# Kernel optimization log

Hardware: AMD Instinct MI355X
Metric: run time of the kernel (lower is better)

Reference implementation:

```python
import jax, jax.numpy as jnp
import numpy as np

B, Lq, Lkv = 4, 1024, 4096
Cq, Ckv, E, NH = 512, 512, 512, 8
HD = E // NH


def setup_inputs() -> dict:
    key = jax.random.key(0)
    ks = jax.random.split(key, 8)
    s = 0.02
    return {
        "Xq": jax.random.normal(ks[0], (B, Lq, Cq), dtype=jnp.float32),
        "Xkv": jax.random.normal(ks[1], (B, Lkv, Ckv), dtype=jnp.float32),
        "mask": jax.random.randint(ks[2], (B, Lq, 1), 0, 2, dtype=jnp.int32),
        "Wq": jax.random.normal(ks[3], (Cq, E), dtype=jnp.float32) * s,
        "bq": jnp.zeros((E,), dtype=jnp.float32),
        "Wkv": jax.random.normal(ks[4], (Ckv, 2 * E), dtype=jnp.float32) * s,
        "bkv": jnp.zeros((2 * E,), dtype=jnp.float32),
        "Wp": jax.random.normal(ks[5], (E, E), dtype=jnp.float32) * s,
        "bp": jnp.zeros((E,), dtype=jnp.float32),
        "attn_pos": jax.random.normal(ks[6], (1, NH, Lq, Lkv), dtype=jnp.float32) * s,
    }


def reference(Xq, Xkv, mask, Wq, bq, Wkv, bkv, Wp, bp, attn_pos):
    scale = HD ** -0.5
    # projections
    Q = (Xq @ Wq + bq).reshape(B, Lq, NH, HD).transpose(0, 2, 1, 3) * scale  # [B,NH,Lq,HD]
    KV = (Xkv @ Wkv + bkv).reshape(B, Lkv, 2, NH, HD)
    K = KV[:, :, 0].transpose(0, 2, 1, 3)  # [B,NH,Lkv,HD]
    V = KV[:, :, 1].transpose(0, 2, 1, 3)
    # scores + learned positional bias
    attn = jnp.einsum('bhqd,bhkd->bhqk', Q, K) + attn_pos  # [B,NH,Lq,Lkv]
    # dummy-column masked softmax (mask: [B,Lq,1], 1=keep row)
    m = mask.astype(attn.dtype)[:, None]           # [B,1,Lq,1]
    attn = attn + (1.0 - m) * (-100.0)             # suppress masked query rows
    dummy = jnp.broadcast_to(jnp.where(m == 0, 100.0, -100.0), (B, NH, Lq, 1))
    attn = jax.nn.softmax(jnp.concatenate([attn, dummy], axis=-1), axis=-1)[..., :Lkv]
    # weighted sum + output projection (dropout = identity in eval)
    out = jnp.einsum('bhqk,bhkd->bhqd', attn, V)
    out = out.transpose(0, 2, 1, 3).reshape(B, Lq, E)
    return out @ Wp + bp
```

## Files before the change

### kernel.cpp

```cpp
#include <hip/hip_runtime.h>

typedef unsigned short u16;
typedef __attribute__((ext_vector_type(8))) short bf16x8;
typedef __attribute__((ext_vector_type(4))) float f32x4;
typedef __attribute__((ext_vector_type(2))) unsigned u32x2;

__device__ __forceinline__ u16 f2bf(float x) {
    union { float f; unsigned u; } v; v.f = x;
    unsigned r = v.u + 0x7FFF + ((v.u >> 16) & 1);
    return (u16)(r >> 16);
}

__device__ __forceinline__ unsigned cvt_pk_bf16(float lo, float hi) {
    unsigned r;
    asm("v_cvt_pk_bf16_f32 %0, %1, %2" : "=v"(r) : "v"(lo), "v"(hi));
    return r;
}

__global__ __launch_bounds__(256) void transpose_w(const float* __restrict__ in,
                                                   u16* __restrict__ out, int R, int C) {
    __shared__ float tile[64][65];
    int r0 = blockIdx.y * 64, c0 = blockIdx.x * 64;
    int tid = threadIdx.x;
#pragma unroll
    for (int j = 0; j < 16; ++j) {
        int e = tid + j * 256;
        int row = e >> 6, col = e & 63;
        tile[row][col] = in[(size_t)(r0 + row) * C + c0 + col];
    }
    __syncthreads();
#pragma unroll
    for (int j = 0; j < 16; ++j) {
        int e = tid + j * 256;
        int row = e >> 6, col = e & 63;
        out[(size_t)(c0 + row) * R + r0 + col] = f2bf(tile[col][row]);
    }
}

__global__ __launch_bounds__(256) void transpose_v(const u16* __restrict__ in,
                                                   u16* __restrict__ out) {
    __shared__ u16 tile[64][65];
    int bh = blockIdx.y;
    int r0 = blockIdx.x * 64;
    const u16* ip = in + (size_t)bh * 4096 * 64;
    u16* op = out + (size_t)bh * 64 * 4096;
    int tid = threadIdx.x;
#pragma unroll
    for (int j = 0; j < 16; ++j) {
        int e = tid + j * 256;
        int row = e >> 6, col = e & 63;
        tile[row][col] = ip[(size_t)(r0 + row) * 64 + col];
    }
    __syncthreads();
#pragma unroll
    for (int j = 0; j < 16; ++j) {
        int e = tid + j * 256;
        int row = e >> 6, col = e & 63;
        op[(size_t)row * 4096 + r0 + col] = tile[col][row];
    }
}

template <int MODE>
__global__ __launch_bounds__(256) void gemm_kernel(const void* __restrict__ Aptr,
                                                   const u16* __restrict__ Bt,
                                                   const float* __restrict__ bias,
                                                   void* __restrict__ Cout,
                                                   void* __restrict__ Cout2,
                                                   int M, int N, int K) {
    __shared__ u16 Al[128][40];
    __shared__ u16 Bl[128][40];
    int tid = threadIdx.x;
    int lane = tid & 63, wid = tid >> 6;
    int wr = wid >> 1, wc = wid & 1;
    int l15 = lane & 15, g = lane >> 4;
    int bm = blockIdx.y, bn = blockIdx.x;

    f32x4 acc[4][4];
#pragma unroll
    for (int m = 0; m < 4; ++m)
#pragma unroll
        for (int n = 0; n < 4; ++n)
#pragma unroll
            for (int j = 0; j < 4; ++j) acc[m][n][j] = 0.f;

    int nK = K >> 5;
    for (int kt = 0; kt < nK; ++kt) {
        __syncthreads();
        if (MODE != 2) {
            const float* A = (const float*)Aptr;
#pragma unroll
            for (int j = 0; j < 4; ++j) {
                int idx4 = tid + j * 256;
                int row = idx4 >> 3, c4 = (idx4 & 7) << 2;
                const float4* p =
                    (const float4*)(A + (size_t)(bm * 128 + row) * K + kt * 32 + c4);
                float4 v = *p;
                u32x2 w = {cvt_pk_bf16(v.x, v.y), cvt_pk_bf16(v.z, v.w)};
                *(u32x2*)&Al[row][c4] = w;
            }
        } else {
            const u16* A = (const u16*)Aptr;
#pragma unroll
            for (int j = 0; j < 2; ++j) {
                int idx8 = tid + j * 256;
                int row = idx8 >> 2, c8 = (idx8 & 3) << 3;
                bf16x8 v = *(const bf16x8*)(A + (size_t)(bm * 128 + row) * K + kt * 32 + c8);
                *(bf16x8*)&Al[row][c8] = v;
            }
        }
#pragma unroll
        for (int j = 0; j < 2; ++j) {
            int idx8 = tid + j * 256;
            int row = idx8 >> 2, c8 = (idx8 & 3) << 3;
            bf16x8 v = *(const bf16x8*)(Bt + (size_t)(bn * 128 + row) * K + kt * 32 + c8);
            *(bf16x8*)&Bl[row][c8] = v;
        }
        __syncthreads();

        bf16x8 af[4], bfr[4];
#pragma unroll
        for (int m = 0; m < 4; ++m) af[m] = *(const bf16x8*)&Al[wr * 64 + m * 16 + l15][g * 8];
#pragma unroll
        for (int n = 0; n < 4; ++n) bfr[n] = *(const bf16x8*)&Bl[wc * 64 + n * 16 + l15][g * 8];
#pragma unroll
        for (int m = 0; m < 4; ++m)
#pragma unroll
            for (int n = 0; n < 4; ++n)
                acc[m][n] =
                    __builtin_amdgcn_mfma_f32_16x16x32_bf16(af[m], bfr[n], acc[m][n], 0, 0, 0);
    }

#pragma unroll
    for (int m = 0; m < 4; ++m)
#pragma unroll
        for (int n = 0; n < 4; ++n)
#pragma unroll
            for (int j = 0; j < 4; ++j) {
                int row = bm * 128 + wr * 64 + m * 16 + g * 4 + j;
                int col = bn * 128 + wc * 64 + n * 16 + l15;
                float v = acc[m][n][j] + bias[col];
                if (MODE == 0) {
                    int b = row >> 10, q = row & 1023, h = col >> 6, d = col & 63;
                    ((u16*)Cout)[(((size_t)((b * 8 + h) * 1024 + q)) << 6) + d] =
                        f2bf(v * 0.125f);
                } else if (MODE == 1) {
                    int b = row >> 12, kv = row & 4095;
                    int d = col & 63;
                    if (col < 512) {
                        int h = col >> 6;
                        ((u16*)Cout)[(((size_t)((b * 8 + h) * 4096 + kv)) << 6) + d] = f2bf(v);
                    } else {
                        int h = (col - 512) >> 6;
                        ((u16*)Cout2)[(((size_t)((b * 8 + h) * 4096 + kv)) << 6) + d] = f2bf(v);
                    }
                } else {
                    ((float*)Cout)[(size_t)row * N + col] = v;
                }
            }
}

__global__ __launch_bounds__(256, 3) void attn_kernel(const u16* __restrict__ Qb,
                                                      const u16* __restrict__ Kb,
                                                      const u16* __restrict__ Vt,
                                                      const float* __restrict__ pos,
                                                      float* __restrict__ Opart,
                                                      float* __restrict__ Lp) {
    __shared__ u16 Klds[64][72];
    __shared__ u16 Vlds[64][72];
    __shared__ u16 Plds[4][32][72];

    int idx = blockIdx.x;
    int bh = idx & 31;
    int zz = idx >> 5;
    int qt = zz & 7, sp = zz >> 3;
    int b = bh >> 3, h = bh & 7;
    int q0 = qt * 128;
    int kvbase = sp * 512;
    int tid = threadIdx.x, lane = tid & 63, wid = tid >> 6;
    int l15 = lane & 15, g = lane >> 4;

    bf16x8 aq[2][2];
#pragma unroll
    for (int m = 0; m < 2; ++m) {
        const u16* qp =
            Qb + (((size_t)((b * 8 + h) * 1024 + q0 + wid * 32 + m * 16 + l15)) << 6) + g * 8;
        aq[m][0] = *(const bf16x8*)(qp);
        aq[m][1] = *(const bf16x8*)(qp + 32);
    }

    f32x4 o[2][4];
    f32x4 lacc[2];
#pragma unroll
    for (int m = 0; m < 2; ++m) {
#pragma unroll
        for (int j = 0; j < 4; ++j) lacc[m][j] = 0.f;
#pragma unroll
        for (int n = 0; n < 4; ++n)
#pragma unroll
            for (int j = 0; j < 4; ++j) o[m][n][j] = 0.f;
    }

    const size_t kbase = ((size_t)(b * 8 + h)) * 4096 * 64;
    const float* posp =
        pos + (size_t)h * 1024 * 4096 + (size_t)(q0 + wid * 32 + g * 4) * 4096 + kvbase;

    int srow = tid >> 3, sc8 = (tid & 7) << 3;

    bf16x8 kr[2], vr[2];
    f32x4 zr[2][4];
#pragma unroll
    for (int j = 0; j < 2; ++j) {
        int row = srow + j * 32;
        kr[j] = *(const bf16x8*)(Kb + kbase + (size_t)(kvbase + row) * 64 + sc8);
        vr[j] = *(const bf16x8*)(Vt + kbase + (size_t)row * 4096 + kvbase + sc8);
    }
#pragma unroll
    for (int m = 0; m < 2; ++m)
#pragma unroll
        for (int n = 0; n < 4; ++n)
#pragma unroll
            for (int j = 0; j < 4; ++j)
                zr[m][n][j] = posp[(size_t)(m * 16 + j) * 4096 + n * 16 + l15];

    const short one_s = (short)0x3F80;
    bf16x8 ones = {one_s, one_s, one_s, one_s, one_s, one_s, one_s, one_s};

    for (int kt = 0; kt < 8; ++kt) {
        __syncthreads();
#pragma unroll
        for (int j = 0; j < 2; ++j) {
            int row = srow + j * 32;
            *(bf16x8*)&Klds[row][sc8] = kr[j];
            *(bf16x8*)&Vlds[row][sc8] = vr[j];
        }
        __syncthreads();

        int knext = (kt + 1) & 7;
#pragma unroll
        for (int j = 0; j < 2; ++j) {
            int row = srow + j * 32;
            kr[j] = *(const bf16x8*)(Kb + kbase + (size_t)(kvbase + knext * 64 + row) * 64 + sc8);
            vr[j] = *(const bf16x8*)(Vt + kbase + (size_t)row * 4096 + kvbase + knext * 64 + sc8);
        }

        f32x4 s[2][4];
        __builtin_amdgcn_s_setprio(1);
#pragma unroll
        for (int n = 0; n < 4; ++n) {
            bf16x8 kb0 = *(const bf16x8*)&Klds[n * 16 + l15][g * 8];
            bf16x8 kb1 = *(const bf16x8*)&Klds[n * 16 + l15][32 + g * 8];
#pragma unroll
            for (int m = 0; m < 2; ++m) {
                f32x4 t =
                    __builtin_amdgcn_mfma_f32_16x16x32_bf16(aq[m][0], kb0, zr[m][n], 0, 0, 0);
                s[m][n] = __builtin_amdgcn_mfma_f32_16x16x32_bf16(aq[m][1], kb1, t, 0, 0, 0);
            }
        }
        __builtin_amdgcn_s_setprio(0);

#pragma unroll
        for (int m = 0; m < 2; ++m)
#pragma unroll
            for (int n = 0; n < 4; ++n)
#pragma unroll
                for (int j = 0; j < 4; ++j)
                    zr[m][n][j] = posp[(size_t)(m * 16 + j) * 4096 + knext * 64 + n * 16 + l15];

#pragma unroll
        for (int m = 0; m < 2; ++m)
#pragma unroll
            for (int n = 0; n < 4; ++n)
#pragma unroll
                for (int j = 0; j < 4; ++j)
                    s[m][n][j] = __builtin_exp2f(fminf(s[m][n][j], 60.f) * 1.44269504f);

#pragma unroll
        for (int m = 0; m < 2; ++m)
#pragma unroll
            for (int j = 0; j < 4; ++j) {
                unsigned w0 = cvt_pk_bf16(s[m][0][j], s[m][1][j]);
                unsigned w1 = cvt_pk_bf16(s[m][2][j], s[m][3][j]);
                int row = m * 16 + g * 4 + j;
                Plds[wid][row][l15] = (u16)w0;
                Plds[wid][row][16 + l15] = (u16)(w0 >> 16);
                Plds[wid][row][32 + l15] = (u16)w1;
                Plds[wid][row][48 + l15] = (u16)(w1 >> 16);
            }
        asm volatile("" ::: "memory");

        bf16x8 pa[2][2];
#pragma unroll
        for (int m = 0; m < 2; ++m) {
            pa[m][0] = *(const bf16x8*)&Plds[wid][m * 16 + l15][g * 8];
            pa[m][1] = *(const bf16x8*)&Plds[wid][m * 16 + l15][32 + g * 8];
        }

        __builtin_amdgcn_s_setprio(1);
#pragma unroll
        for (int n = 0; n < 4; ++n) {
            bf16x8 vb0 = *(const bf16x8*)&Vlds[n * 16 + l15][g * 8];
            bf16x8 vb1 = *(const bf16x8*)&Vlds[n * 16 + l15][32 + g * 8];
#pragma unroll
            for (int m = 0; m < 2; ++m) {
                o[m][n] = __builtin_amdgcn_mfma_f32_16x16x32_bf16(pa[m][0], vb0, o[m][n], 0, 0, 0);
                o[m][n] = __builtin_amdgcn_mfma_f32_16x16x32_bf16(pa[m][1], vb1, o[m][n], 0, 0, 0);
            }
        }
#pragma unroll
        for (int m = 0; m < 2; ++m) {
            lacc[m] = __builtin_amdgcn_mfma_f32_16x16x32_bf16(pa[m][0], ones, lacc[m], 0, 0, 0);
            lacc[m] = __builtin_amdgcn_mfma_f32_16x16x32_bf16(pa[m][1], ones, lacc[m], 0, 0, 0);
        }
        __builtin_amdgcn_s_setprio(0);
    }

    int obase = (sp * 32 + bh) * 1024;
#pragma unroll
    for (int m = 0; m < 2; ++m)
#pragma unroll
        for (int j = 0; j < 4; ++j) {
            int row = q0 + wid * 32 + m * 16 + g * 4 + j;
#pragma unroll
            for (int n = 0; n < 4; ++n)
                Opart[((size_t)(obase + row)) * 64 + n * 16 + l15] = o[m][n][j];
            if (l15 == 0) Lp[obase + row] = lacc[m][j];
        }
}

__global__ __launch_bounds__(256) void attn_combine(const float* __restrict__ Opart,
                                                    const float* __restrict__ Lp,
                                                    const int* __restrict__ mask,
                                                    u16* __restrict__ AO) {
    int tid = threadIdx.x;
    int d = tid & 63;
    int r = blockIdx.x * 4 + (tid >> 6);
    int bh = r >> 10, q = r & 1023;
    int b = bh >> 3, h = bh & 7;

    float L = 0.f, val = 0.f;
#pragma unroll
    for (int s2 = 0; s2 < 8; ++s2) {
        size_t rr = (size_t)(s2 * 32 + bh) * 1024 + q;
        L += Lp[rr];
        val += Opart[rr * 64 + d];
    }
    float res = mask[b * 1024 + q] ? (val / L) : 0.f;
    AO[((size_t)(b * 1024 + q)) * 512 + h * 64 + d] = f2bf(res);
}

extern "C" void kernel_launch(void* const* d_in, const int* in_sizes, int n_in,
                              void* d_out, int out_size, void* d_ws, size_t ws_size,
                              hipStream_t stream) {
    const float* Xq = (const float*)d_in[0];
    const float* Xkv = (const float*)d_in[1];
    const int* mask = (const int*)d_in[2];
    const float* Wq = (const float*)d_in[3];
    const float* bq = (const float*)d_in[4];
    const float* Wkv = (const float*)d_in[5];
    const float* bkv = (const float*)d_in[6];
    const float* Wp = (const float*)d_in[7];
    const float* bp = (const float*)d_in[8];
    const float* pos = (const float*)d_in[9];
    float* out = (float*)d_out;

    char* ws = (char*)d_ws;
    u16* WqT = (u16*)(ws);
    u16* WkvT = (u16*)(ws + 524288);
    u16* WpT = (u16*)(ws + 1572864);
    u16* Qb = (u16*)(ws + 2097152);
    u16* Kb = (u16*)(ws + 6291456);
    u16* Vt = (u16*)(ws + 23068672);
    u16* AO = (u16*)(ws + 39845888);
    float* Opart = (float*)(ws + 44040192);
    u16* Vtm = (u16*)(ws + 44040192);
    float* Lp = (float*)(ws + 111149056);

    transpose_w<<<dim3(8, 8), 256, 0, stream>>>(Wq, WqT, 512, 512);
    transpose_w<<<dim3(16, 8), 256, 0, stream>>>(Wkv, WkvT, 512, 1024);
    transpose_w<<<dim3(8, 8), 256, 0, stream>>>(Wp, WpT, 512, 512);
    gemm_kernel<0><<<dim3(4, 32), 256, 0, stream>>>(Xq, WqT, bq, Qb, nullptr, 4096, 512, 512);
    gemm_kernel<1><<<dim3(8, 128), 256, 0, stream>>>(Xkv, WkvT, bkv, Kb, Vtm, 16384, 1024, 512);
    transpose_v<<<dim3(64, 32), 256, 0, stream>>>(Vtm, Vt);
    attn_kernel<<<dim3(2048), 256, 0, stream>>>(Qb, Kb, Vt, pos, Opart, Lp);
    attn_combine<<<dim3(8192), 256, 0, stream>>>(Opart, Lp, mask, AO);
    gemm_kernel<2><<<dim3(4, 32), 256, 0, stream>>>(AO, WpT, bp, out, nullptr, 4096, 512, 512);
}
```

Measured before the change: 206.6 us.

## Pre-convert inputs to bf16, use direct global-to-LDS GEMM loads, transpose attention score layout

Adds a pre-pass that converts Xq and Xkv to bf16. The projection GEMMs now load A and B tiles straight into LDS with global_load_lds, using a 64-wide K step. The attention kernel swaps the MFMA operands so scores come out transposed, which allows vectorized f32x4 loads of the positional bias and a smaller P staging buffer written with packed stores. The log2e factor is folded into the Q scale and the bias, and occupancy is raised to 4 blocks per CU. This trades extra conversion kernels and workspace traffic for cheaper GEMM staging and fewer attention memory instructions. It risks LDS bank conflicts because the unpadded 64-wide tiles are read back with strided row accesses.

```diff
diff --git a/kernel.cpp b/kernel.cpp
--- a/kernel.cpp
+++ b/kernel.cpp
@@ -4,6 +4,7 @@
 typedef __attribute__((ext_vector_type(8))) short bf16x8;
 typedef __attribute__((ext_vector_type(4))) float f32x4;
 typedef __attribute__((ext_vector_type(2))) unsigned u32x2;
+typedef __attribute__((ext_vector_type(4))) unsigned u32x4;
 
 __device__ __forceinline__ u16 f2bf(float x) {
     union { float f; unsigned u; } v; v.f = x;
@@ -15,6 +16,21 @@
     unsigned r;
     asm("v_cvt_pk_bf16_f32 %0, %1, %2" : "=v"(r) : "v"(lo), "v"(hi));
     return r;
+}
+
+__device__ __forceinline__ void gl_lds16(const u16* g, u16* l) {
+    __builtin_amdgcn_global_load_lds((const __attribute__((address_space(1))) void*)g,
+                                     (__attribute__((address_space(3))) void*)l, 16, 0, 0);
+}
+
+__global__ __launch_bounds__(256) void conv_bf16(const float* __restrict__ in,
+                                                 u16* __restrict__ out) {
+    size_t i = ((size_t)blockIdx.x * 256 + threadIdx.x) * 8;
+    const float4* p = (const float4*)(in + i);
+    float4 a = p[0], b = p[1];
+    u32x4 w = {cvt_pk_bf16(a.x, a.y), cvt_pk_bf16(a.z, a.w),
+               cvt_pk_bf16(b.x, b.y), cvt_pk_bf16(b.z, b.w)};
+    *(u32x4*)(out + i) = w;
 }
 
 __global__ __launch_bounds__(256) void transpose_w(const float* __restrict__ in,
@@ -61,19 +77,20 @@
 }
 
 template <int MODE>
-__global__ __launch_bounds__(256) void gemm_kernel(const void* __restrict__ Aptr,
+__global__ __launch_bounds__(256) void gemm_kernel(const u16* __restrict__ A,
                                                    const u16* __restrict__ Bt,
                                                    const float* __restrict__ bias,
                                                    void* __restrict__ Cout,
                                                    void* __restrict__ Cout2,
                                                    int M, int N, int K) {
-    __shared__ u16 Al[128][40];
-    __shared__ u16 Bl[128][40];
+    __shared__ u16 Al[128][64];
+    __shared__ u16 Bl[128][64];
     int tid = threadIdx.x;
     int lane = tid & 63, wid = tid >> 6;
     int wr = wid >> 1, wc = wid & 1;
     int l15 = lane & 15, g = lane >> 4;
     int bm = blockIdx.y, bn = blockIdx.x;
+    int ldr = lane >> 3, ldc = (lane & 7) << 3;
 
     f32x4 acc[4][4];
 #pragma unroll
@@ -83,51 +100,34 @@
 #pragma unroll
             for (int j = 0; j < 4; ++j) acc[m][n][j] = 0.f;
 
-    int nK = K >> 5;
+    int nK = K >> 6;
     for (int kt = 0; kt < nK; ++kt) {
         __syncthreads();
-        if (MODE != 2) {
-            const float* A = (const float*)Aptr;
-#pragma unroll
-            for (int j = 0; j < 4; ++j) {
-                int idx4 = tid + j * 256;
-                int row = idx4 >> 3, c4 = (idx4 & 7) << 2;
-                const float4* p =
-                    (const float4*)(A + (size_t)(bm * 128 + row) * K + kt * 32 + c4);
-                float4 v = *p;
-                u32x2 w = {cvt_pk_bf16(v.x, v.y), cvt_pk_bf16(v.z, v.w)};
-                *(u32x2*)&Al[row][c4] = w;
-            }
-        } else {
-            const u16* A = (const u16*)Aptr;
-#pragma unroll
-            for (int j = 0; j < 2; ++j) {
-                int idx8 = tid + j * 256;
-                int row = idx8 >> 2, c8 = (idx8 & 3) << 3;
-                bf16x8 v = *(const bf16x8*)(A + (size_t)(bm * 128 + row) * K + kt * 32 + c8);
-                *(bf16x8*)&Al[row][c8] = v;
-            }
-        }
-#pragma unroll
-        for (int j = 0; j < 2; ++j) {
-            int idx8 = tid + j * 256;
-            int row = idx8 >> 2, c8 = (idx8 & 3) << 3;
-            bf16x8 v = *(const bf16x8*)(Bt + (size_t)(bn * 128 + row) * K + kt * 32 + c8);
-            *(bf16x8*)&Bl[row][c8] = v;
+#pragma unroll
+        for (int i = 0; i < 4; ++i) {
+            int c = wid * 4 + i;
+            int row = c * 8 + ldr;
+            gl_lds16(A + (size_t)(bm * 128 + row) * K + kt * 64 + ldc, &Al[0][0] + c * 512);
+            gl_lds16(Bt + (size_t)(bn * 128 + row) * K + kt * 64 + ldc, &Bl[0][0] + c * 512);
         }
         __syncthreads();
 
-        bf16x8 af[4], bfr[4];
-#pragma unroll
-        for (int m = 0; m < 4; ++m) af[m] = *(const bf16x8*)&Al[wr * 64 + m * 16 + l15][g * 8];
-#pragma unroll
-        for (int n = 0; n < 4; ++n) bfr[n] = *(const bf16x8*)&Bl[wc * 64 + n * 16 + l15][g * 8];
-#pragma unroll
-        for (int m = 0; m < 4; ++m)
+#pragma unroll
+        for (int kk = 0; kk < 2; ++kk) {
+            bf16x8 af[4], bfr[4];
+#pragma unroll
+            for (int m = 0; m < 4; ++m)
+                af[m] = *(const bf16x8*)&Al[wr * 64 + m * 16 + l15][kk * 32 + g * 8];
 #pragma unroll
             for (int n = 0; n < 4; ++n)
-                acc[m][n] =
-                    __builtin_amdgcn_mfma_f32_16x16x32_bf16(af[m], bfr[n], acc[m][n], 0, 0, 0);
+                bfr[n] = *(const bf16x8*)&Bl[wc * 64 + n * 16 + l15][kk * 32 + g * 8];
+#pragma unroll
+            for (int m = 0; m < 4; ++m)
+#pragma unroll
+                for (int n = 0; n < 4; ++n)
+                    acc[m][n] =
+                        __builtin_amdgcn_mfma_f32_16x16x32_bf16(af[m], bfr[n], acc[m][n], 0, 0, 0);
+        }
     }
 
 #pragma unroll
@@ -142,7 +142,7 @@
                 if (MODE == 0) {
                     int b = row >> 10, q = row & 1023, h = col >> 6, d = col & 63;
                     ((u16*)Cout)[(((size_t)((b * 8 + h) * 1024 + q)) << 6) + d] =
-                        f2bf(v * 0.125f);
+                        f2bf(v * 0.18033688011112042f);
                 } else if (MODE == 1) {
                     int b = row >> 12, kv = row & 4095;
                     int d = col & 63;
@@ -159,7 +159,7 @@
             }
 }
 
-__global__ __launch_bounds__(256, 3) void attn_kernel(const u16* __restrict__ Qb,
+__global__ __launch_bounds__(256, 4) void attn_kernel(const u16* __restrict__ Qb,
                                                       const u16* __restrict__ Kb,
                                                       const u16* __restrict__ Vt,
                                                       const float* __restrict__ pos,
@@ -167,7 +167,7 @@
                                                       float* __restrict__ Lp) {
     __shared__ u16 Klds[64][72];
     __shared__ u16 Vlds[64][72];
-    __shared__ u16 Plds[4][32][72];
+    __shared__ u16 Plds[4][16][72];
 
     int idx = blockIdx.x;
     int bh = idx & 31;
@@ -202,7 +202,7 @@
 
     const size_t kbase = ((size_t)(b * 8 + h)) * 4096 * 64;
     const float* posp =
-        pos + (size_t)h * 1024 * 4096 + (size_t)(q0 + wid * 32 + g * 4) * 4096 + kvbase;
+        pos + (size_t)h * 1024 * 4096 + (size_t)(q0 + wid * 32 + l15) * 4096 + kvbase;
 
     int srow = tid >> 3, sc8 = (tid & 7) << 3;
 
@@ -217,10 +217,11 @@
 #pragma unroll
     for (int m = 0; m < 2; ++m)
 #pragma unroll
-        for (int n = 0; n < 4; ++n)
-#pragma unroll
-            for (int j = 0; j < 4; ++j)
-                zr[m][n][j] = posp[(size_t)(m * 16 + j) * 4096 + n * 16 + l15];
+        for (int n = 0; n < 4; ++n) {
+            zr[m][n] = *(const f32x4*)(posp + (size_t)m * 16 * 4096 + n * 16 + g * 4);
+#pragma unroll
+            for (int j = 0; j < 4; ++j) zr[m][n][j] *= 1.44269504f;
+        }
 
     const short one_s = (short)0x3F80;
     bf16x8 ones = {one_s, one_s, one_s, one_s, one_s, one_s, one_s, one_s};
@@ -252,8 +253,8 @@
 #pragma unroll
             for (int m = 0; m < 2; ++m) {
                 f32x4 t =
-                    __builtin_amdgcn_mfma_f32_16x16x32_bf16(aq[m][0], kb0, zr[m][n], 0, 0, 0);
-                s[m][n] = __builtin_amdgcn_mfma_f32_16x16x32_bf16(aq[m][1], kb1, t, 0, 0, 0);
+                    __builtin_amdgcn_mfma_f32_16x16x32_bf16(kb0, aq[m][0], zr[m][n], 0, 0, 0);
+                s[m][n] = __builtin_amdgcn_mfma_f32_16x16x32_bf16(kb1, aq[m][1], t, 0, 0, 0);
             }
         }
         __builtin_amdgcn_s_setprio(0);
@@ -261,38 +262,35 @@
 #pragma unroll
         for (int m = 0; m < 2; ++m)
 #pragma unroll
+            for (int n = 0; n < 4; ++n) {
+                zr[m][n] = *(const f32x4*)(posp + (size_t)m * 16 * 4096 + knext * 64 + n * 16 +
+                                           g * 4);
+#pragma unroll
+                for (int j = 0; j < 4; ++j) zr[m][n][j] *= 1.44269504f;
+            }
+
+#pragma unroll
+        for (int m = 0; m < 2; ++m)
+#pragma unroll
             for (int n = 0; n < 4; ++n)
 #pragma unroll
                 for (int j = 0; j < 4; ++j)
-                    zr[m][n][j] = posp[(size_t)(m * 16 + j) * 4096 + knext * 64 + n * 16 + l15];
-
-#pragma unroll
-        for (int m = 0; m < 2; ++m)
-#pragma unroll
-            for (int n = 0; n < 4; ++n)
-#pragma unroll
-                for (int j = 0; j < 4; ++j)
-                    s[m][n][j] = __builtin_exp2f(fminf(s[m][n][j], 60.f) * 1.44269504f);
-
-#pragma unroll
-        for (int m = 0; m < 2; ++m)
-#pragma unroll
-            for (int j = 0; j < 4; ++j) {
-                unsigned w0 = cvt_pk_bf16(s[m][0][j], s[m][1][j]);
-                unsigned w1 = cvt_pk_bf16(s[m][2][j], s[m][3][j]);
-                int row = m * 16 + g * 4 + j;
-                Plds[wid][row][l15] = (u16)w0;
-                Plds[wid][row][16 + l15] = (u16)(w0 >> 16);
-                Plds[wid][row][32 + l15] = (u16)w1;
-                Plds[wid][row][48 + l15] = (u16)(w1 >> 16);
-            }
-        asm volatile("" ::: "memory");
+                    s[m][n][j] = __builtin_exp2f(fminf(s[m][n][j], 80.f));
 
         bf16x8 pa[2][2];
 #pragma unroll
         for (int m = 0; m < 2; ++m) {
-            pa[m][0] = *(const bf16x8*)&Plds[wid][m * 16 + l15][g * 8];
-            pa[m][1] = *(const bf16x8*)&Plds[wid][m * 16 + l15][32 + g * 8];
+#pragma unroll
+            for (int n = 0; n < 4; ++n) {
+                u32x2 w;
+                w.x = cvt_pk_bf16(s[m][n][0], s[m][n][1]);
+                w.y = cvt_pk_bf16(s[m][n][2], s[m][n][3]);
+                *(u32x2*)&Plds[wid][l15][n * 16 + g * 4] = w;
+            }
+            asm volatile("" ::: "memory");
+            pa[m][0] = *(const bf16x8*)&Plds[wid][l15][g * 8];
+            pa[m][1] = *(const bf16x8*)&Plds[wid][l15][32 + g * 8];
+            asm volatile("" ::: "memory");
         }
 
         __builtin_amdgcn_s_setprio(1);
@@ -372,14 +370,18 @@
     u16* Vt = (u16*)(ws + 23068672);
     u16* AO = (u16*)(ws + 39845888);
     float* Opart = (float*)(ws + 44040192);
-    u16* Vtm = (u16*)(ws + 44040192);
+    u16* Xkvb = (u16*)(ws + 44040192);
+    u16* Vtm = (u16*)(ws + 60817408);
+    u16* Xqb = (u16*)(ws + 77594624);
     float* Lp = (float*)(ws + 111149056);
 
+    conv_bf16<<<dim3(1024), 256, 0, stream>>>(Xq, Xqb);
+    conv_bf16<<<dim3(4096), 256, 0, stream>>>(Xkv, Xkvb);
     transpose_w<<<dim3(8, 8), 256, 0, stream>>>(Wq, WqT, 512, 512);
     transpose_w<<<dim3(16, 8), 256, 0, stream>>>(Wkv, WkvT, 512, 1024);
     transpose_w<<<dim3(8, 8), 256, 0, stream>>>(Wp, WpT, 512, 512);
-    gemm_kernel<0><<<dim3(4, 32), 256, 0, stream>>>(Xq, WqT, bq, Qb, nullptr, 4096, 512, 512);
-    gemm_kernel<1><<<dim3(8, 128), 256, 0, stream>>>(Xkv, WkvT, bkv, Kb, Vtm, 16384, 1024, 512);
+    gemm_kernel<0><<<dim3(4, 32), 256, 0, stream>>>(Xqb, WqT, bq, Qb, nullptr, 4096, 512, 512);
+    gemm_kernel<1><<<dim3(8, 128), 256, 0, stream>>>(Xkvb, WkvT, bkv, Kb, Vtm, 16384, 1024, 512);
     transpose_v<<<dim3(64, 32), 256, 0, stream>>>(Vtm, Vt);
     attn_kernel<<<dim3(2048), 256, 0, stream>>>(Qb, Kb, Vt, pos, Opart, Lp);
     attn_combine<<<dim3(8192), 256, 0, stream>>>(Opart, Lp, mask, AO);
```

Result: slower. 324.3 us (+56.9%).
